# Performance work log

Hardware: AMD Instinct MI355X
Metric: run time of the kernel (lower is better)

The kernel has to match this reference:

```python
import jax, jax.numpy as jnp
import numpy as np

N, S, L, K, D = 8, 2048, 8, 1024, 1024


def setup_inputs() -> dict:
    key = jax.random.key(0)
    k1, k2 = jax.random.split(key)
    x = jax.random.randint(k1, (N, S, L), 0, K, dtype=jnp.int64)
    weight = jax.random.normal(k2, (L, K, D), dtype=jnp.float32)
    return {"x": x, "weight": weight}


def reference(x, weight):
    # Original: one_hot(x.transpose(1,-1), K) then einsum 'l k d, n l s k -> n s d'
    # which is exactly out[n,s,d] = sum_l weight[l, x[n,s,l], d].
    L_ = weight.shape[0]
    lvl = jnp.arange(L_)  # (L,)
    # Advanced indexing: weight[l, x[n,s,l]] -> (N, S, L, D), then sum over levels.
    gathered = weight[lvl[None, None, :], x]  # (N, S, L, D)
    return gathered.sum(axis=2)  # (N, S, D)
```

## Files before the change

### kernel.cpp

```cpp
#include <hip/hip_runtime.h>
#include <hip/hip_bf16.h>
#include <hip/hip_fp16.h>


#define NS      (8 * 2048)
#define LVL     8
#define KK      1024
#define DD      1024
#define NCH     8
#define DCH     (DD / NCH)
#define ROWSPB  32
#define THREADS 256

typedef _Float16 half8 __attribute__((ext_vector_type(8)));
typedef float    f32x4 __attribute__((ext_vector_type(4)));
typedef float    f32x8 __attribute__((ext_vector_type(8)));

__global__ __launch_bounds__(THREADS) void convert_w_kernel(
    const float* __restrict__ w, _Float16* __restrict__ wh)
{
    const size_t i = ((size_t)blockIdx.x * THREADS + threadIdx.x) * 8;
    const f32x8 v = *reinterpret_cast<const f32x8*>(w + i);
    const half8 h = __builtin_convertvector(v, half8);
    *reinterpret_cast<half8*>(wh + i) = h;
}

__global__ __launch_bounds__(THREADS, 4) void multi_embedding_kernel(
    const int* __restrict__ x,
    const _Float16* __restrict__ wh,
    float* __restrict__ out)
{
    const int chunk = blockIdx.x & (NCH - 1);
    const int nsg   = blockIdx.x >> 3;
    const int tid   = threadIdx.x;
    const int ns0   = nsg * ROWSPB;

    __shared__ int sidx[ROWSPB * LVL];
    sidx[tid] = x[(size_t)ns0 * LVL + tid];
    __syncthreads();
    const int4* s4 = reinterpret_cast<const int4*>(sidx);

    const int lane = tid & 15;
    const int rg   = tid >> 4;
    const _Float16* wl = wh + (size_t)chunk * DCH + (size_t)lane * 8;

    const int rowA = rg;
    const int rowB = rg + 16;

    const int4 a0 = s4[rowA * 2], a1 = s4[rowA * 2 + 1];
    const int4 b0 = s4[rowB * 2], b1 = s4[rowB * 2 + 1];
    const int idxA[LVL] = { a0.x, a0.y, a0.z, a0.w, a1.x, a1.y, a1.z, a1.w };
    const int idxB[LVL] = { b0.x, b0.y, b0.z, b0.w, b1.x, b1.y, b1.z, b1.w };

    half8 accA = *reinterpret_cast<const half8*>(
        wl + ((size_t)idxA[0] << 10));
    half8 accB = *reinterpret_cast<const half8*>(
        wl + ((size_t)idxB[0] << 10));
#pragma unroll
    for (int l = 1; l < LVL; ++l) {
        const half8 vA = *reinterpret_cast<const half8*>(
            wl + ((size_t)((l << 10) + idxA[l]) << 10));
        const half8 vB = *reinterpret_cast<const half8*>(
            wl + ((size_t)((l << 10) + idxB[l]) << 10));
        accA += vA;
        accB += vB;
    }

    const f32x8 fA = __builtin_convertvector(accA, f32x8);
    const f32x8 fB = __builtin_convertvector(accB, f32x8);
    const f32x4 fA_lo = __builtin_shufflevector(fA, fA, 0, 1, 2, 3);
    const f32x4 fA_hi = __builtin_shufflevector(fA, fA, 4, 5, 6, 7);
    const f32x4 fB_lo = __builtin_shufflevector(fB, fB, 0, 1, 2, 3);
    const f32x4 fB_hi = __builtin_shufflevector(fB, fB, 4, 5, 6, 7);

    float* oA = out + (size_t)(ns0 + rowA) * DD + (size_t)chunk * DCH + (size_t)lane * 8;
    float* oB = out + (size_t)(ns0 + rowB) * DD + (size_t)chunk * DCH + (size_t)lane * 8;
    __builtin_nontemporal_store(fA_lo, reinterpret_cast<f32x4*>(oA));
    __builtin_nontemporal_store(fA_hi, reinterpret_cast<f32x4*>(oA) + 1);
    __builtin_nontemporal_store(fB_lo, reinterpret_cast<f32x4*>(oB));
    __builtin_nontemporal_store(fB_hi, reinterpret_cast<f32x4*>(oB) + 1);
}

extern "C" void kernel_launch(void* const* d_in, const int* in_sizes, int n_in,
                              void* d_out, int out_size, void* d_ws, size_t ws_size,
                              hipStream_t stream) {
    const int*   x = (const int*)d_in[0];
    const float* w = (const float*)d_in[1];
    float*     out = (float*)d_out;
    _Float16*   wh = (_Float16*)d_ws;

    convert_w_kernel<<<dim3((LVL * KK * DD) / (THREADS * 8)), dim3(THREADS), 0, stream>>>(w, wh);

    multi_embedding_kernel<<<dim3((NS / ROWSPB) * NCH), dim3(THREADS), 0, stream>>>(x, wh, out);
}
```

Baseline: 109.0 us.

## Gather fp32 weights directly, dropping the fp16 conversion pre-pass

Removes the separate kernel that converted the whole weight table to fp16 and instead gathers fp32 rows directly in the embedding kernel. Each thread now handles 4 rows with 4-float vectors rather than 2 rows with 8-half vectors, and indices are read from shared memory per level. This saves a full read and write pass over the 32 MB weight table and one launch, and accumulates in fp32 for better accuracy. In exchange the gather reads twice as many bytes per row, though the table may fit in the large last-level cache.

New measurement: 107.6 us. Within noise of the previous version (-1.3%).

```diff
diff --git a/kernel.cpp b/kernel.cpp
--- a/kernel.cpp
+++ b/kernel.cpp
@@ -1,6 +1,4 @@
 #include <hip/hip_runtime.h>
-#include <hip/hip_bf16.h>
-#include <hip/hip_fp16.h>
 
 
 #define NS      (8 * 2048)
@@ -12,22 +10,11 @@
 #define ROWSPB  32
 #define THREADS 256
 
-typedef _Float16 half8 __attribute__((ext_vector_type(8)));
-typedef float    f32x4 __attribute__((ext_vector_type(4)));
-typedef float    f32x8 __attribute__((ext_vector_type(8)));
+typedef float f32x4 __attribute__((ext_vector_type(4)));
 
-__global__ __launch_bounds__(THREADS) void convert_w_kernel(
-    const float* __restrict__ w, _Float16* __restrict__ wh)
-{
-    const size_t i = ((size_t)blockIdx.x * THREADS + threadIdx.x) * 8;
-    const f32x8 v = *reinterpret_cast<const f32x8*>(w + i);
-    const half8 h = __builtin_convertvector(v, half8);
-    *reinterpret_cast<half8*>(wh + i) = h;
-}
-
-__global__ __launch_bounds__(THREADS, 4) void multi_embedding_kernel(
+__global__ __launch_bounds__(THREADS, 4) void multi_embedding_f32_kernel(
     const int* __restrict__ x,
-    const _Float16* __restrict__ wh,
+    const float* __restrict__ w,
     float* __restrict__ out)
 {
     const int chunk = blockIdx.x & (NCH - 1);
@@ -38,47 +25,36 @@
     __shared__ int sidx[ROWSPB * LVL];
     sidx[tid] = x[(size_t)ns0 * LVL + tid];
     __syncthreads();
-    const int4* s4 = reinterpret_cast<const int4*>(sidx);
 
-    const int lane = tid & 15;
-    const int rg   = tid >> 4;
-    const _Float16* wl = wh + (size_t)chunk * DCH + (size_t)lane * 8;
+    const int lane = tid & 31;
+    const int rg   = tid >> 5;
 
-    const int rowA = rg;
-    const int rowB = rg + 16;
+    const float* wl = w + (size_t)chunk * DCH + (size_t)lane * 4;
 
-    const int4 a0 = s4[rowA * 2], a1 = s4[rowA * 2 + 1];
-    const int4 b0 = s4[rowB * 2], b1 = s4[rowB * 2 + 1];
-    const int idxA[LVL] = { a0.x, a0.y, a0.z, a0.w, a1.x, a1.y, a1.z, a1.w };
-    const int idxB[LVL] = { b0.x, b0.y, b0.z, b0.w, b1.x, b1.y, b1.z, b1.w };
+    const int rows[4] = { rg, rg + 8, rg + 16, rg + 24 };
 
-    half8 accA = *reinterpret_cast<const half8*>(
-        wl + ((size_t)idxA[0] << 10));
-    half8 accB = *reinterpret_cast<const half8*>(
-        wl + ((size_t)idxB[0] << 10));
+    f32x4 acc[4];
+#pragma unroll
+    for (int r = 0; r < 4; ++r) {
+        const int idx0 = sidx[rows[r] * LVL + 0];
+        acc[r] = *reinterpret_cast<const f32x4*>(wl + ((size_t)idx0 << 10));
+    }
 #pragma unroll
     for (int l = 1; l < LVL; ++l) {
-        const half8 vA = *reinterpret_cast<const half8*>(
-            wl + ((size_t)((l << 10) + idxA[l]) << 10));
-        const half8 vB = *reinterpret_cast<const half8*>(
-            wl + ((size_t)((l << 10) + idxB[l]) << 10));
-        accA += vA;
-        accB += vB;
+#pragma unroll
+        for (int r = 0; r < 4; ++r) {
+            const int idx = sidx[rows[r] * LVL + l];
+            acc[r] += *reinterpret_cast<const f32x4*>(
+                wl + ((size_t)((l << 10) + idx) << 10));
+        }
     }
 
-    const f32x8 fA = __builtin_convertvector(accA, f32x8);
-    const f32x8 fB = __builtin_convertvector(accB, f32x8);
-    const f32x4 fA_lo = __builtin_shufflevector(fA, fA, 0, 1, 2, 3);
-    const f32x4 fA_hi = __builtin_shufflevector(fA, fA, 4, 5, 6, 7);
-    const f32x4 fB_lo = __builtin_shufflevector(fB, fB, 0, 1, 2, 3);
-    const f32x4 fB_hi = __builtin_shufflevector(fB, fB, 4, 5, 6, 7);
-
-    float* oA = out + (size_t)(ns0 + rowA) * DD + (size_t)chunk * DCH + (size_t)lane * 8;
-    float* oB = out + (size_t)(ns0 + rowB) * DD + (size_t)chunk * DCH + (size_t)lane * 8;
-    __builtin_nontemporal_store(fA_lo, reinterpret_cast<f32x4*>(oA));
-    __builtin_nontemporal_store(fA_hi, reinterpret_cast<f32x4*>(oA) + 1);
-    __builtin_nontemporal_store(fB_lo, reinterpret_cast<f32x4*>(oB));
-    __builtin_nontemporal_store(fB_hi, reinterpret_cast<f32x4*>(oB) + 1);
+#pragma unroll
+    for (int r = 0; r < 4; ++r) {
+        float* o = out + (size_t)(ns0 + rows[r]) * DD
+                 + (size_t)chunk * DCH + (size_t)lane * 4;
+        __builtin_nontemporal_store(acc[r], reinterpret_cast<f32x4*>(o));
+    }
 }
 
 extern "C" void kernel_launch(void* const* d_in, const int* in_sizes, int n_in,
@@ -87,9 +63,6 @@
     const int*   x = (const int*)d_in[0];
     const float* w = (const float*)d_in[1];
     float*     out = (float*)d_out;
-    _Float16*   wh = (_Float16*)d_ws;
 
-    convert_w_kernel<<<dim3((LVL * KK * DD) / (THREADS * 8)), dim3(THREADS), 0, stream>>>(w, wh);
-
-    multi_embedding_kernel<<<dim3((NS / ROWSPB) * NCH), dim3(THREADS), 0, stream>>>(x, wh, out);
+    multi_embedding_f32_kernel<<<dim3((NS / ROWSPB) * NCH), dim3(THREADS), 0, stream>>>(x, w, out);
 }
```
